# Optimization experiments

Hardware: AMD Instinct MI355X
Metric: run time of the kernel (lower is better)

## Reference

```python
import jax, jax.numpy as jnp
import numpy as np

Q_HEADS, KV_HEADS, DIMS = 16, 4, 1024
HEAD_DIM = DIMS // Q_HEADS          # 64
GROUPS = Q_HEADS // KV_HEADS        # 4
ROPE_BASE = 10000.0


def rope(x):
    # x: (..., s, d) -- standard interleaved rotary embedding, base 10000
    s, d = x.shape[-2], x.shape[-1]
    inv_freq = 1.0 / (ROPE_BASE ** (jnp.arange(0, d, 2, dtype=jnp.float32) / d))
    ang = jnp.arange(s, dtype=jnp.float32)[:, None] * inv_freq[None, :]  # (s, d/2)
    cos, sin = jnp.cos(ang), jnp.sin(ang)
    x1, x2 = x[..., 0::2], x[..., 1::2]
    out = jnp.stack([x1 * cos - x2 * sin, x1 * sin + x2 * cos], axis=-1)
    return out.reshape(x.shape).astype(x.dtype)


def setup_inputs() -> dict:
    key = jax.random.key(0)
    k1, k2, k3, k4, k5, k6 = jax.random.split(key, 6)
    B, S, E = 4, 2048, 1024
    q = jax.random.normal(k1, (B, S, E), dtype=jnp.float32)
    kv = jax.random.normal(k2, (B, S, E), dtype=jnp.float32)
    sc = 1.0 / np.sqrt(E)
    Wq = jax.random.normal(k3, (E, Q_HEADS, HEAD_DIM), dtype=jnp.float32) * sc
    Wk = jax.random.normal(k4, (E, KV_HEADS, HEAD_DIM), dtype=jnp.float32) * sc
    Wv = jax.random.normal(k5, (E, KV_HEADS, HEAD_DIM), dtype=jnp.float32) * sc
    Wo = jax.random.normal(k6, (HEAD_DIM, E), dtype=jnp.float32) / np.sqrt(HEAD_DIM)
    return {"q": q, "kv": kv, "Wq": Wq, "Wk": Wk, "Wv": Wv, "Wo": Wo}


def reference(q, kv, Wq, Wk, Wv, Wo):
    B, S, E = q.shape
    qh = jnp.einsum('bse,ehd->bshd', q, Wq)    # (B,S,Q_HEADS,hd)
    kh = jnp.einsum('bse,ehd->bshd', kv, Wk)   # (B,S,KV_HEADS,hd)
    vh = jnp.einsum('bse,ehd->bshd', kv, Wv)
    # rearrange '... s (h g) d -> ... g h s d' with g=GROUPS (h = KV_HEADS outer)
    qh = qh.reshape(B, S, KV_HEADS, GROUPS, HEAD_DIM).transpose(0, 3, 2, 1, 4)  # (B,g,h,S,d)
    kh = kh.transpose(0, 2, 1, 3)  # (B,h,S,d)
    vh = vh.transpose(0, 2, 1, 3)  # (B,h,S,d)
    qh = rope(qh)
    kh = rope(kh)
    # NOTE: sums over group axis g (faithful to original einsum)
    scores = jnp.einsum('bghsd,bhad->bhsa', qh, kh)
    attn = jax.nn.softmax(scores / (HEAD_DIM ** 0.5), axis=-1)
    out = jnp.einsum('bhsa,bhad->bhsd', attn, vh)  # (B,h,S,d)
    out = out.mean(axis=1)                          # mean over kv heads -> (B,S,d)
    return out @ Wo                                 # (B,S,E)
```

## Files before the change

### kernel.cpp

```cpp
#include <hip/hip_runtime.h>
#include <math.h>

#define SS 2048
#define EE 1024

using bf16x8 = __attribute__((ext_vector_type(8))) short;
using f32x4  = __attribute__((ext_vector_type(4))) float;

__device__ inline short f2bf(float x) {
    unsigned u = __builtin_bit_cast(unsigned, x);
    return (short)((u + 0x7fffu + ((u >> 16) & 1u)) >> 16);
}
__device__ inline short f2bf_r(float x) {
    return (short)((__builtin_bit_cast(unsigned, x) + 0x8000u) >> 16);
}
__device__ inline unsigned pk_bf16(float a, float b) {
    unsigned ua = __builtin_bit_cast(unsigned, a) + 0x8000u;
    unsigned ub = __builtin_bit_cast(unsigned, b) + 0x8000u;
    return __builtin_amdgcn_perm(ub, ua, 0x07060302u);
}

__global__ __launch_bounds__(256) void prep_weights(const float* __restrict__ Wq,
                                                    const float* __restrict__ Wk,
                                                    const float* __restrict__ Wv,
                                                    const float* __restrict__ Wo,
                                                    short* __restrict__ Wall,
                                                    short* __restrict__ Wo4,
                                                    float2* __restrict__ RT) {
    int idx = blockIdx.x * 256 + threadIdx.x;
    int c = idx >> 10, e = idx & 1023;
    int h = c >> 6, d = c & 63;
    const float* p = Wq + (size_t)e * 1024 + h * 256 + d;
    Wall[(size_t)c * 1024 + e] = f2bf(0.18033688011112042f * (p[0] + p[64] + p[128] + p[192]));
    Wall[(size_t)(256 + c) * 1024 + e] = f2bf(Wk[(size_t)e * 256 + c]);
    Wall[(size_t)(512 + c) * 1024 + e] = f2bf(Wv[(size_t)e * 256 + c]);
    Wo4[(size_t)e * 256 + c] = f2bf(0.25f * Wo[(size_t)d * 1024 + e]);
    if (idx < 65536) {
        int s = idx >> 5, ii = idx & 31;
        float freq = __expf(-(float)ii * (9.210340371976184f / 32.0f));
        float sn, cs;
        sincosf((float)s * freq, &sn, &cs);
        RT[idx] = (float2){cs, sn};
    }
}

__global__ __launch_bounds__(256) void proj_kernel(const float* __restrict__ q,
                                                   const float* __restrict__ kv,
                                                   const short* __restrict__ Wall,
                                                   const float2* __restrict__ RT,
                                                   short* __restrict__ Qb,
                                                   short* __restrict__ Kb,
                                                   short* __restrict__ Vt) {
    __shared__ alignas(16) short As[128][72];
    __shared__ alignas(16) short Bs[64][72];
    int tid = threadIdx.x;
    int wave = tid >> 6, lane = tid & 63, quad = lane >> 4, c16 = lane & 15;
    int wm = wave >> 1, wn = wave & 1;
    int m0 = blockIdx.x * 128, n0 = blockIdx.y * 64;
    const float* A = (n0 < 256) ? q : kv;

    f32x4 acc[4][2];
    #pragma unroll
    for (int i = 0; i < 4; i++)
        #pragma unroll
        for (int j = 0; j < 2; j++) acc[i][j] = (f32x4){0.f, 0.f, 0.f, 0.f};

    for (int k0 = 0; k0 < 1024; k0 += 64) {
        #pragma unroll
        for (int i = 0; i < 8; i++) {
            int id = i * 256 + tid, r = id >> 4, ch = id & 15;
            float4 v = *(const float4*)&A[(size_t)(m0 + r) * 1024 + k0 + ch * 4];
            uint2 u;
            u.x = pk_bf16(v.x, v.y);
            u.y = pk_bf16(v.z, v.w);
            *(uint2*)&As[r][ch * 4] = u;
        }
        #pragma unroll
        for (int i = 0; i < 2; i++) {
            int id = i * 256 + tid, r = id >> 3, ch = id & 7;
            *(int4*)&Bs[r][ch * 8] =
                *(const int4*)&Wall[(size_t)(n0 + r) * 1024 + k0 + ch * 8];
        }
        __syncthreads();
        #pragma unroll
        for (int ks = 0; ks < 64; ks += 32) {
            bf16x8 af[4], bfr[2];
            #pragma unroll
            for (int mt = 0; mt < 4; mt++)
                af[mt] = *(const bf16x8*)&As[wm * 64 + mt * 16 + c16][ks + quad * 8];
            #pragma unroll
            for (int nt = 0; nt < 2; nt++)
                bfr[nt] = *(const bf16x8*)&Bs[wn * 32 + nt * 16 + c16][ks + quad * 8];
            #pragma unroll
            for (int mt = 0; mt < 4; mt++)
                #pragma unroll
                for (int nt = 0; nt < 2; nt++)
                    acc[mt][nt] = __builtin_amdgcn_mfma_f32_16x16x32_bf16(
                        af[mt], bfr[nt], acc[mt][nt], 0, 0, 0);
        }
        __syncthreads();
    }
    if (n0 < 512) {
        #pragma unroll
        for (int mt = 0; mt < 4; mt++) {
            #pragma unroll
            for (int nt = 0; nt < 2; nt++) {
                int cl = wn * 32 + nt * 16 + c16;
                int ii = ((n0 + cl) & 63) >> 1;
                float sgn = (lane & 1) ? 1.0f : -1.0f;
                f32x4 v = acc[mt][nt];
                #pragma unroll
                for (int r = 0; r < 4; r++) {
                    int rl = wm * 64 + mt * 16 + quad * 4 + r;
                    float2 cs = RT[((m0 + rl) & (SS - 1)) * 32 + ii];
                    float other = __shfl_xor(v[r], 1);
                    As[rl][cl] = f2bf_r(v[r] * cs.x + sgn * cs.y * other);
                }
            }
        }
        __syncthreads();
        short* dstb = (n0 < 256) ? Qb : Kb;
        int nc0 = n0 & 255;
        #pragma unroll
        for (int i = 0; i < 4; i++) {
            int id = i * 256 + tid, r = id >> 3, ch = id & 7;
            *(int4*)&dstb[(size_t)(m0 + r) * 256 + nc0 + ch * 8] =
                *(const int4*)&As[r][ch * 8];
        }
    } else {
        short (*Lt)[136] = (short(*)[136])&As[0][0];
        #pragma unroll
        for (int mt = 0; mt < 4; mt++) {
            #pragma unroll
            for (int nt = 0; nt < 2; nt++) {
                int cl = wn * 32 + nt * 16 + c16;
                int sl = wm * 64 + mt * 16 + quad * 4;
                f32x4 v = acc[mt][nt];
                uint2 u;
                u.x = pk_bf16(v[0], v[1]);
                u.y = pk_bf16(v[2], v[3]);
                *(uint2*)&Lt[cl][sl] = u;
            }
        }
        __syncthreads();
        int b = m0 >> 11, s0 = m0 & (SS - 1), c0 = n0 - 512;
        #pragma unroll
        for (int i = 0; i < 4; i++) {
            int id = i * 256 + tid, c = id >> 4, ch = id & 15;
            *(int4*)&Vt[((size_t)(b * 256 + c0 + c)) * SS + s0 + ch * 8] =
                *(const int4*)&Lt[c][ch * 8];
        }
    }
}

__global__ __launch_bounds__(512, 4) void attn_kernel(const short* __restrict__ Qb,
                                                      const short* __restrict__ Kb,
                                                      const short* __restrict__ Vt,
                                                      short* __restrict__ Ob) {
    __shared__ alignas(16) short Qs[64][72];
    __shared__ alignas(16) short Ps2[64][72];
    __shared__ alignas(16) short Ks[2][64][72];
    __shared__ alignas(16) short Vs[2][64][72];
    int tid = threadIdx.x;
    int wave = tid >> 6, lane = tid & 63, quad = lane >> 4, c16 = lane & 15;
    int rq = wave & 3, kh = wave >> 2;
    int qt = blockIdx.x, bh = blockIdx.y;
    int q0 = qt * 64;
    size_t qkbase = (size_t)(bh >> 2) * SS * 256 + (bh & 3) * 64;
    size_t vtbase = (size_t)(bh * 64) * SS;

    {
        int r = tid >> 3, ch = tid & 7;
        *(int4*)&Qs[r][ch * 8] = *(const int4*)&Qb[qkbase + (size_t)(q0 + r) * 256 + ch * 8];
    }
    __syncthreads();
    bf16x8 aq0 = *(const bf16x8*)&Qs[rq * 16 + c16][quad * 8];
    bf16x8 aq1 = *(const bf16x8*)&Qs[rq * 16 + c16][32 + quad * 8];
    short (*Ps)[72] = (kh == 0) ? (short (*)[72])Qs[rq * 16] : (short (*)[72])Ps2[rq * 16];

    float lsum[4] = {0.f, 0.f, 0.f, 0.f};
    f32x4 o[4];
    #pragma unroll
    for (int dt = 0; dt < 4; dt++) o[dt] = (f32x4){0.f, 0.f, 0.f, 0.f};

    int sr = tid >> 3, sch = tid & 7;
    for (int kt = 0; kt < 16; kt++) {
        int a0 = kt * 64;
        __syncthreads();
        *(int4*)&Ks[0][sr][sch * 8] =
            *(const int4*)&Kb[qkbase + (size_t)(a0 + sr) * 256 + sch * 8];
        *(int4*)&Ks[1][sr][sch * 8] =
            *(const int4*)&Kb[qkbase + (size_t)(1024 + a0 + sr) * 256 + sch * 8];
        *(int4*)&Vs[0][sr][sch * 8] =
            *(const int4*)&Vt[vtbase + (size_t)sr * SS + a0 + sch * 8];
        *(int4*)&Vs[1][sr][sch * 8] =
            *(const int4*)&Vt[vtbase + (size_t)sr * SS + 1024 + a0 + sch * 8];
        __syncthreads();
        f32x4 sv[4];
        #pragma unroll
        for (int nt = 0; nt < 4; nt++) sv[nt] = (f32x4){0.f, 0.f, 0.f, 0.f};
        #pragma unroll
        for (int nt = 0; nt < 4; nt++) {
            bf16x8 bk0 = *(const bf16x8*)&Ks[kh][nt * 16 + c16][quad * 8];
            bf16x8 bk1 = *(const bf16x8*)&Ks[kh][nt * 16 + c16][32 + quad * 8];
            sv[nt] = __builtin_amdgcn_mfma_f32_16x16x32_bf16(aq0, bk0, sv[nt], 0, 0, 0);
            sv[nt] = __builtin_amdgcn_mfma_f32_16x16x32_bf16(aq1, bk1, sv[nt], 0, 0, 0);
        }
        #pragma unroll
        for (int nt = 0; nt < 4; nt++)
            #pragma unroll
            for (int r = 0; r < 4; r++) sv[nt][r] = __builtin_exp2f(sv[nt][r]);
        #pragma unroll
        for (int r = 0; r < 4; r++)
            lsum[r] += (sv[0][r] + sv[1][r]) + (sv[2][r] + sv[3][r]);
        #pragma unroll
        for (int nt = 0; nt < 4; nt++)
            #pragma unroll
            for (int r = 0; r < 4; r++)
                Ps[quad * 4 + r][nt * 16 + c16] = f2bf_r(sv[nt][r]);
        #pragma unroll
        for (int ks = 0; ks < 64; ks += 32) {
            bf16x8 ap = *(const bf16x8*)&Ps[c16][ks + quad * 8];
            #pragma unroll
            for (int dt = 0; dt < 4; dt++) {
                bf16x8 bv = *(const bf16x8*)&Vs[kh][dt * 16 + c16][ks + quad * 8];
                o[dt] = __builtin_amdgcn_mfma_f32_16x16x32_bf16(ap, bv, o[dt], 0, 0, 0);
            }
        }
    }
    #pragma unroll
    for (int off = 1; off < 16; off <<= 1)
        #pragma unroll
        for (int r = 0; r < 4; r++) lsum[r] += __shfl_xor(lsum[r], off);

    __syncthreads();
    float (*Ox)[68] = (float (*)[68])&Ks[0][0][0];
    float* Lx = (float*)&Vs[0][0][0];
    short (*Ot)[72] = (short (*)[72])&Vs[1][0][0];
    int base = rq * 16 + quad * 4;
    if (wave >= 4) {
        #pragma unroll
        for (int dt = 0; dt < 4; dt++)
            #pragma unroll
            for (int r = 0; r < 4; r++)
                Ox[base + r][dt * 16 + c16] = o[dt][r];
        if (c16 == 0)
            #pragma unroll
            for (int r = 0; r < 4; r++) Lx[base + r] = lsum[r];
    }
    __syncthreads();
    if (wave < 4) {
        #pragma unroll
        for (int r = 0; r < 4; r++) {
            float rl = __builtin_amdgcn_rcpf(lsum[r] + Lx[base + r]);
            #pragma unroll
            for (int dt = 0; dt < 4; dt++)
                Ot[base + r][dt * 16 + c16] =
                    f2bf_r((o[dt][r] + Ox[base + r][dt * 16 + c16]) * rl);
        }
    }
    __syncthreads();
    {
        int r = tid >> 3, ch = tid & 7;
        int b = bh >> 2, h = bh & 3;
        *(int4*)&Ob[((size_t)(b * SS + q0 + r)) * 256 + h * 64 + ch * 8] =
            *(const int4*)&Ot[r][ch * 8];
    }
}

__global__ __launch_bounds__(256) void outproj_kernel(const short* __restrict__ Ob,
                                                      const short* __restrict__ Wo4,
                                                      float* __restrict__ out) {
    __shared__ alignas(16) short As[128][72];
    __shared__ alignas(16) short Bs[128][72];
    int tid = threadIdx.x;
    int wave = tid >> 6, lane = tid & 63, quad = lane >> 4, c16 = lane & 15;
    int wm = wave >> 1, wn = wave & 1;
    int m0 = blockIdx.x * 128, n0 = blockIdx.y * 128;

    f32x4 acc[4][4];
    #pragma unroll
    for (int i = 0; i < 4; i++)
        #pragma unroll
        for (int j = 0; j < 4; j++) acc[i][j] = (f32x4){0.f, 0.f, 0.f, 0.f};

    for (int k0 = 0; k0 < 256; k0 += 64) {
        #pragma unroll
        for (int i = 0; i < 4; i++) {
            int id = i * 256 + tid, r = id >> 3, ch = id & 7;
            *(int4*)&As[r][ch * 8] =
                *(const int4*)&Ob[(size_t)(m0 + r) * 256 + k0 + ch * 8];
            *(int4*)&Bs[r][ch * 8] =
                *(const int4*)&Wo4[(size_t)(n0 + r) * 256 + k0 + ch * 8];
        }
        __syncthreads();
        #pragma unroll
        for (int ks = 0; ks < 64; ks += 32) {
            bf16x8 af[4], bfr[4];
            #pragma unroll
            for (int mt = 0; mt < 4; mt++)
                af[mt] = *(const bf16x8*)&As[wm * 64 + mt * 16 + c16][ks + quad * 8];
            #pragma unroll
            for (int nt = 0; nt < 4; nt++)
                bfr[nt] = *(const bf16x8*)&Bs[wn * 64 + nt * 16 + c16][ks + quad * 8];
            #pragma unroll
            for (int mt = 0; mt < 4; mt++)
                #pragma unroll
                for (int nt = 0; nt < 4; nt++)
                    acc[mt][nt] = __builtin_amdgcn_mfma_f32_16x16x32_bf16(
                        af[mt], bfr[nt], acc[mt][nt], 0, 0, 0);
        }
        __syncthreads();
    }
    #pragma unroll
    for (int mt = 0; mt < 4; mt++)
        #pragma unroll
        for (int nt = 0; nt < 4; nt++) {
            int col = n0 + wn * 64 + nt * 16 + c16;
            int rowb = m0 + wm * 64 + mt * 16 + quad * 4;
            #pragma unroll
            for (int r = 0; r < 4; r++)
                out[(size_t)(rowb + r) * 1024 + col] = acc[mt][nt][r];
        }
}

extern "C" void kernel_launch(void* const* d_in, const int* in_sizes, int n_in,
                              void* d_out, int out_size, void* d_ws, size_t ws_size,
                              hipStream_t stream) {
    const float* q  = (const float*)d_in[0];
    const float* kv = (const float*)d_in[1];
    const float* Wq = (const float*)d_in[2];
    const float* Wk = (const float*)d_in[3];
    const float* Wv = (const float*)d_in[4];
    const float* Wo = (const float*)d_in[5];
    float* out = (float*)d_out;

    short* Qb    = (short*)d_ws;
    short* Kb    = Qb + 2097152;
    short* Vt    = Kb + 2097152;
    short* Wall  = Vt + 2097152;
    short* Wo4   = Wall + 786432;
    float2* RT   = (float2*)(Wo4 + 262144);
    short* Ob    = (short*)(RT + 65536);

    prep_weights<<<1024, 256, 0, stream>>>(Wq, Wk, Wv, Wo, Wall, Wo4, RT);

    proj_kernel<<<dim3(64, 12), 256, 0, stream>>>(q, kv, Wall, RT, Qb, Kb, Vt);

    attn_kernel<<<dim3(32, 16), 512, 0, stream>>>(Qb, Kb, Vt, Ob);

    outproj_kernel<<<dim3(64, 8), 256, 0, stream>>>(Ob, Wo4, out);
}
```

Before: 207.8 us.

## Shrink projection GEMM tiles and prefetch K/V tiles into registers in attention

Makes the projection kernel tiles smaller (64x64 instead of 128x64) and the output projection tiles smaller (128x64 instead of 128x128), doubling the grid sizes. On a GPU with many CUs the old grids were only a few hundred blocks, so this aims at better occupancy. The attention kernel now loads the next K/V tile from global memory into registers while the current tile is being computed, hiding global load latency. The cost is less data reuse per block, so more global and LDS traffic per FLOP, plus extra registers held for the prefetch.

```diff
diff --git a/kernel.cpp b/kernel.cpp
--- a/kernel.cpp
+++ b/kernel.cpp
@@ -51,23 +51,20 @@
                                                    short* __restrict__ Qb,
                                                    short* __restrict__ Kb,
                                                    short* __restrict__ Vt) {
-    __shared__ alignas(16) short As[128][72];
+    __shared__ alignas(16) short As[64][72];
     __shared__ alignas(16) short Bs[64][72];
     int tid = threadIdx.x;
     int wave = tid >> 6, lane = tid & 63, quad = lane >> 4, c16 = lane & 15;
-    int wm = wave >> 1, wn = wave & 1;
-    int m0 = blockIdx.x * 128, n0 = blockIdx.y * 64;
+    int m0 = blockIdx.x * 64, n0 = blockIdx.y * 64;
     const float* A = (n0 < 256) ? q : kv;
 
-    f32x4 acc[4][2];
-    #pragma unroll
-    for (int i = 0; i < 4; i++)
-        #pragma unroll
-        for (int j = 0; j < 2; j++) acc[i][j] = (f32x4){0.f, 0.f, 0.f, 0.f};
+    f32x4 acc[4];
+    #pragma unroll
+    for (int j = 0; j < 4; j++) acc[j] = (f32x4){0.f, 0.f, 0.f, 0.f};
 
     for (int k0 = 0; k0 < 1024; k0 += 64) {
         #pragma unroll
-        for (int i = 0; i < 8; i++) {
+        for (int i = 0; i < 4; i++) {
             int id = i * 256 + tid, r = id >> 4, ch = id & 15;
             float4 v = *(const float4*)&A[(size_t)(m0 + r) * 1024 + k0 + ch * 4];
             uint2 u;
@@ -84,69 +81,56 @@
         __syncthreads();
         #pragma unroll
         for (int ks = 0; ks < 64; ks += 32) {
-            bf16x8 af[4], bfr[2];
-            #pragma unroll
-            for (int mt = 0; mt < 4; mt++)
-                af[mt] = *(const bf16x8*)&As[wm * 64 + mt * 16 + c16][ks + quad * 8];
-            #pragma unroll
-            for (int nt = 0; nt < 2; nt++)
-                bfr[nt] = *(const bf16x8*)&Bs[wn * 32 + nt * 16 + c16][ks + quad * 8];
-            #pragma unroll
-            for (int mt = 0; mt < 4; mt++)
-                #pragma unroll
-                for (int nt = 0; nt < 2; nt++)
-                    acc[mt][nt] = __builtin_amdgcn_mfma_f32_16x16x32_bf16(
-                        af[mt], bfr[nt], acc[mt][nt], 0, 0, 0);
+            bf16x8 af = *(const bf16x8*)&As[wave * 16 + c16][ks + quad * 8];
+            #pragma unroll
+            for (int nt = 0; nt < 4; nt++) {
+                bf16x8 bfr = *(const bf16x8*)&Bs[nt * 16 + c16][ks + quad * 8];
+                acc[nt] = __builtin_amdgcn_mfma_f32_16x16x32_bf16(af, bfr, acc[nt], 0, 0, 0);
+            }
         }
         __syncthreads();
     }
     if (n0 < 512) {
         #pragma unroll
-        for (int mt = 0; mt < 4; mt++) {
-            #pragma unroll
-            for (int nt = 0; nt < 2; nt++) {
-                int cl = wn * 32 + nt * 16 + c16;
-                int ii = ((n0 + cl) & 63) >> 1;
-                float sgn = (lane & 1) ? 1.0f : -1.0f;
-                f32x4 v = acc[mt][nt];
-                #pragma unroll
-                for (int r = 0; r < 4; r++) {
-                    int rl = wm * 64 + mt * 16 + quad * 4 + r;
-                    float2 cs = RT[((m0 + rl) & (SS - 1)) * 32 + ii];
-                    float other = __shfl_xor(v[r], 1);
-                    As[rl][cl] = f2bf_r(v[r] * cs.x + sgn * cs.y * other);
-                }
+        for (int nt = 0; nt < 4; nt++) {
+            int cl = nt * 16 + c16;
+            int ii = cl >> 1;
+            float sgn = (lane & 1) ? 1.0f : -1.0f;
+            f32x4 v = acc[nt];
+            #pragma unroll
+            for (int r = 0; r < 4; r++) {
+                int rl = wave * 16 + quad * 4 + r;
+                float2 cs = RT[((m0 + rl) & (SS - 1)) * 32 + ii];
+                float other = __shfl_xor(v[r], 1);
+                As[rl][cl] = f2bf_r(v[r] * cs.x + sgn * cs.y * other);
             }
         }
         __syncthreads();
         short* dstb = (n0 < 256) ? Qb : Kb;
         int nc0 = n0 & 255;
         #pragma unroll
-        for (int i = 0; i < 4; i++) {
+        for (int i = 0; i < 2; i++) {
             int id = i * 256 + tid, r = id >> 3, ch = id & 7;
             *(int4*)&dstb[(size_t)(m0 + r) * 256 + nc0 + ch * 8] =
                 *(const int4*)&As[r][ch * 8];
         }
     } else {
-        short (*Lt)[136] = (short(*)[136])&As[0][0];
-        #pragma unroll
-        for (int mt = 0; mt < 4; mt++) {
-            #pragma unroll
-            for (int nt = 0; nt < 2; nt++) {
-                int cl = wn * 32 + nt * 16 + c16;
-                int sl = wm * 64 + mt * 16 + quad * 4;
-                f32x4 v = acc[mt][nt];
-                uint2 u;
-                u.x = pk_bf16(v[0], v[1]);
-                u.y = pk_bf16(v[2], v[3]);
-                *(uint2*)&Lt[cl][sl] = u;
-            }
+        short (*Lt)[72] = As;
+        #pragma unroll
+        for (int nt = 0; nt < 4; nt++) {
+            int cl = nt * 16 + c16;
+            int sl = wave * 16 + quad * 4;
+            f32x4 v = acc[nt];
+            uint2 u;
+            u.x = pk_bf16(v[0], v[1]);
+            u.y = pk_bf16(v[2], v[3]);
+            *(uint2*)&Lt[cl][sl] = u;
         }
         __syncthreads();
         int b = m0 >> 11, s0 = m0 & (SS - 1), c0 = n0 - 512;
         #pragma unroll
-        for (int i = 0; i < 4; i++) {
-            int id = i * 256 + tid, c = id >> 4, ch = id & 15;
+        for (int i = 0; i < 2; i++) {
+            int id = i * 256 + tid, c = id >> 3, ch = id & 7;
             *(int4*)&Vt[((size_t)(b * 256 + c0 + c)) * SS + s0 + ch * 8] =
                 *(const int4*)&Lt[c][ch * 8];
         }
@@ -184,17 +168,24 @@
     for (int dt = 0; dt < 4; dt++) o[dt] = (f32x4){0.f, 0.f, 0.f, 0.f};
 
     int sr = tid >> 3, sch = tid & 7;
+    int4 kr0 = *(const int4*)&Kb[qkbase + (size_t)sr * 256 + sch * 8];
+    int4 kr1 = *(const int4*)&Kb[qkbase + (size_t)(1024 + sr) * 256 + sch * 8];
+    int4 vr0 = *(const int4*)&Vt[vtbase + (size_t)sr * SS + sch * 8];
+    int4 vr1 = *(const int4*)&Vt[vtbase + (size_t)sr * SS + 1024 + sch * 8];
+
     for (int kt = 0; kt < 16; kt++) {
-        int a0 = kt * 64;
-        __syncthreads();
-        *(int4*)&Ks[0][sr][sch * 8] =
-            *(const int4*)&Kb[qkbase + (size_t)(a0 + sr) * 256 + sch * 8];
-        *(int4*)&Ks[1][sr][sch * 8] =
-            *(const int4*)&Kb[qkbase + (size_t)(1024 + a0 + sr) * 256 + sch * 8];
-        *(int4*)&Vs[0][sr][sch * 8] =
-            *(const int4*)&Vt[vtbase + (size_t)sr * SS + a0 + sch * 8];
-        *(int4*)&Vs[1][sr][sch * 8] =
-            *(const int4*)&Vt[vtbase + (size_t)sr * SS + 1024 + a0 + sch * 8];
+        __syncthreads();
+        *(int4*)&Ks[0][sr][sch * 8] = kr0;
+        *(int4*)&Ks[1][sr][sch * 8] = kr1;
+        *(int4*)&Vs[0][sr][sch * 8] = vr0;
+        *(int4*)&Vs[1][sr][sch * 8] = vr1;
+        if (kt < 15) {
+            int a1 = (kt + 1) * 64;
+            kr0 = *(const int4*)&Kb[qkbase + (size_t)(a1 + sr) * 256 + sch * 8];
+            kr1 = *(const int4*)&Kb[qkbase + (size_t)(1024 + a1 + sr) * 256 + sch * 8];
+            vr0 = *(const int4*)&Vt[vtbase + (size_t)sr * SS + a1 + sch * 8];
+            vr1 = *(const int4*)&Vt[vtbase + (size_t)sr * SS + 1024 + a1 + sch * 8];
+        }
         __syncthreads();
         f32x4 sv[4];
         #pragma unroll
@@ -272,15 +263,14 @@
                                                       const short* __restrict__ Wo4,
                                                       float* __restrict__ out) {
     __shared__ alignas(16) short As[128][72];
-    __shared__ alignas(16) short Bs[128][72];
+    __shared__ alignas(16) short Bs[64][72];
     int tid = threadIdx.x;
     int wave = tid >> 6, lane = tid & 63, quad = lane >> 4, c16 = lane & 15;
-    int wm = wave >> 1, wn = wave & 1;
-    int m0 = blockIdx.x * 128, n0 = blockIdx.y * 128;
-
-    f32x4 acc[4][4];
-    #pragma unroll
-    for (int i = 0; i < 4; i++)
+    int m0 = blockIdx.x * 128, n0 = blockIdx.y * 64;
+
+    f32x4 acc[2][4];
+    #pragma unroll
+    for (int i = 0; i < 2; i++)
         #pragma unroll
         for (int j = 0; j < 4; j++) acc[i][j] = (f32x4){0.f, 0.f, 0.f, 0.f};
 
@@ -290,21 +280,25 @@
             int id = i * 256 + tid, r = id >> 3, ch = id & 7;
             *(int4*)&As[r][ch * 8] =
                 *(const int4*)&Ob[(size_t)(m0 + r) * 256 + k0 + ch * 8];
+        }
+        #pragma unroll
+        for (int i = 0; i < 2; i++) {
+            int id = i * 256 + tid, r = id >> 3, ch = id & 7;
             *(int4*)&Bs[r][ch * 8] =
                 *(const int4*)&Wo4[(size_t)(n0 + r) * 256 + k0 + ch * 8];
         }
         __syncthreads();
         #pragma unroll
         for (int ks = 0; ks < 64; ks += 32) {
-            bf16x8 af[4], bfr[4];
-            #pragma unroll
-            for (int mt = 0; mt < 4; mt++)
-                af[mt] = *(const bf16x8*)&As[wm * 64 + mt * 16 + c16][ks + quad * 8];
+            bf16x8 af[2], bfr[4];
+            #pragma unroll
+            for (int mt = 0; mt < 2; mt++)
+                af[mt] = *(const bf16x8*)&As[wave * 32 + mt * 16 + c16][ks + quad * 8];
             #pragma unroll
             for (int nt = 0; nt < 4; nt++)
-                bfr[nt] = *(const bf16x8*)&Bs[wn * 64 + nt * 16 + c16][ks + quad * 8];
-            #pragma unroll
-            for (int mt = 0; mt < 4; mt++)
+                bfr[nt] = *(const bf16x8*)&Bs[nt * 16 + c16][ks + quad * 8];
+            #pragma unroll
+            for (int mt = 0; mt < 2; mt++)
                 #pragma unroll
                 for (int nt = 0; nt < 4; nt++)
                     acc[mt][nt] = __builtin_amdgcn_mfma_f32_16x16x32_bf16(
@@ -313,11 +307,11 @@
         __syncthreads();
     }
     #pragma unroll
-    for (int mt = 0; mt < 4; mt++)
+    for (int mt = 0; mt < 2; mt++)
         #pragma unroll
         for (int nt = 0; nt < 4; nt++) {
-            int col = n0 + wn * 64 + nt * 16 + c16;
-            int rowb = m0 + wm * 64 + mt * 16 + quad * 4;
+            int col = n0 + nt * 16 + c16;
+            int rowb = m0 + wave * 32 + mt * 16 + quad * 4;
             #pragma unroll
             for (int r = 0; r < 4; r++)
                 out[(size_t)(rowb + r) * 1024 + col] = acc[mt][nt][r];
@@ -345,9 +339,9 @@
 
     prep_weights<<<1024, 256, 0, stream>>>(Wq, Wk, Wv, Wo, Wall, Wo4, RT);
 
-    proj_kernel<<<dim3(64, 12), 256, 0, stream>>>(q, kv, Wall, RT, Qb, Kb, Vt);
+    proj_kernel<<<dim3(128, 12), 256, 0, stream>>>(q, kv, Wall, RT, Qb, Kb, Vt);
 
     attn_kernel<<<dim3(32, 16), 512, 0, stream>>>(Qb, Kb, Vt, Ob);
 
-    outproj_kernel<<<dim3(64, 8), 256, 0, stream>>>(Ob, Wo4, out);
-}
+    outproj_kernel<<<dim3(64, 16), 256, 0, stream>>>(Ob, Wo4, out);
+}
```

Result: faster. 199.4 us (-4.0%).
